# Kernel optimization log

Hardware: AMD Instinct MI355X
Metric: run time of the kernel (lower is better)

## Reference

```python
import jax, jax.numpy as jnp
import numpy as np

DIM = 512
HID = 512
H = 8
HD = HID // H
RB_HID = 64
COORD = 3


def setup_inputs() -> dict:
    key = jax.random.key(0)
    ks = jax.random.split(key, 12)
    B, Nq, Nk = 2, 1024, 2048
    s = 0.02
    return {
        "q_in": jax.random.normal(ks[0], (B, Nq, DIM), jnp.float32),
        "kv_in": jax.random.normal(ks[1], (B, Nk, DIM), jnp.float32),
        "q_coords": jax.random.normal(ks[2], (B, Nq, COORD), jnp.float32),
        "kv_coords": jax.random.normal(ks[3], (B, Nk, COORD), jnp.float32),
        "Wq": jax.random.normal(ks[4], (DIM, HID), jnp.float32) * s,
        "Wk": jax.random.normal(ks[5], (DIM, HID), jnp.float32) * s,
        "Wv": jax.random.normal(ks[6], (DIM, HID), jnp.float32) * s,
        "Wo": jax.random.normal(ks[7], (HID, DIM), jnp.float32) * s,
        "W1": jax.random.normal(ks[8], (1, RB_HID), jnp.float32) * s,
        "b1": jnp.zeros((RB_HID,), jnp.float32),
        "W2": jax.random.normal(ks[9], (RB_HID, H), jnp.float32) * s,
        "b2": jnp.zeros((H,), jnp.float32),
    }


def reference(q_in, kv_in, q_coords, kv_coords, Wq, Wk, Wv, Wo, W1, b1, W2, b2):
    B, Nq, _ = q_in.shape
    Nk = kv_in.shape[1]
    # projections -> [B, H, N, HD]
    q = (q_in @ Wq).reshape(B, Nq, H, HD).transpose(0, 2, 1, 3)
    k = (kv_in @ Wk).reshape(B, Nk, H, HD).transpose(0, 2, 1, 3)
    v = (kv_in @ Wv).reshape(B, Nk, H, HD).transpose(0, 2, 1, 3)
    # pairwise Euclidean distance [B, Nq, Nk]
    diff = q_coords[:, :, None, :] - kv_coords[:, None, :, :]
    d = jnp.sqrt(jnp.sum(diff * diff, axis=-1))
    # 2-layer MLP on distance -> per-head bias [B, H, Nq, Nk]
    h = jax.nn.silu(d[..., None] * W1[0] + b1)  # [B,Nq,Nk,RB_HID]
    bias = (h @ W2 + b2).transpose(0, 3, 1, 2)  # [B,H,Nq,Nk]
    scale = HD ** -0.5
    logits = jnp.einsum("bhqd,bhkd->bhqk", q, k) * scale + bias
    attn = jax.nn.softmax(logits, axis=-1)
    out = jnp.einsum("bhqk,bhkd->bhqd", attn, v)
    out = out.transpose(0, 2, 1, 3).reshape(B, Nq, HID)
    return out @ Wo
```

## Files before the change

kernel.cpp:

```cpp
#include <hip/hip_runtime.h>
#include <hip/hip_bf16.h>
#include <math.h>

typedef short bf16x8 __attribute__((ext_vector_type(8)));
typedef float f32x4 __attribute__((ext_vector_type(4)));
typedef unsigned short u16;
typedef unsigned int u32;

#define NH 8
#define BB 2
#define NQ 1024
#define NK 2048
#define NSPLIT 8
#define M2CONST 6.4921250
#define SC2 0.18033688f
#define LS 68

#define MFMA16(a, b, c) __builtin_amdgcn_mfma_f32_16x16x32_bf16(a, b, c, 0, 0, 0)

__device__ __constant__ double XN_D[6] = {251.63850576500074, 218.50966799187810,
                                          161.12883777312265, 94.871162226877350,
                                          37.490330081221910, 4.3614942349992570};

static __device__ __forceinline__ u32 bfr(float x) {
  u32 u = __builtin_bit_cast(u32, x);
  return u + 0x7FFFu + ((u >> 16) & 1u);
}
static __device__ __forceinline__ u32 pk2(float lo, float hi) {
  return (bfr(lo) >> 16) | (bfr(hi) & 0xFFFF0000u);
}
static __device__ __forceinline__ u16 bfs(float x) { return (u16)(bfr(x) >> 16); }

__global__ __launch_bounds__(256) void setup_kernel(
    const float* __restrict__ Wq, const float* __restrict__ Wk,
    const float* __restrict__ Wv, const float* __restrict__ Wo,
    u16* __restrict__ Tq, u16* __restrict__ Tk,
    u16* __restrict__ Tv, u16* __restrict__ To,
    const float* __restrict__ W1, const float* __restrict__ b1,
    const float* __restrict__ W2, const float* __restrict__ b2,
    float* __restrict__ polyc,
    const float* __restrict__ kc, u16* __restrict__ keg,
    const float* __restrict__ q_in, const float* __restrict__ kv_in,
    u16* __restrict__ qb, u16* __restrict__ kvb) {
  const int blk = blockIdx.x, t = threadIdx.x;
  if (blk >= 273) {
    int gi = (blk - 273) * 256 + t;
    const float* src; u16* dst; size_t off;
    if (gi < 131072) { src = q_in; dst = qb; off = (size_t)gi * 8; }
    else             { src = kv_in; dst = kvb; off = (size_t)(gi - 131072) * 8; }
    float4 a = *(const float4*)(src + off);
    float4 b = *(const float4*)(src + off + 4);
    uint4 o;
    o.x = pk2(a.x, a.y); o.y = pk2(a.z, a.w);
    o.z = pk2(b.x, b.y); o.w = pk2(b.z, b.w);
    *(uint4*)(dst + off) = o;
  } else if (blk < 256) {
    __shared__ u16 tile[64][65];
    const float* W; u16* Wt;
    switch (blk >> 6) {
      case 0: W = Wq; Wt = Tq; break;
      case 1: W = Wk; Wt = Tk; break;
      case 2: W = Wv; Wt = Tv; break;
      default: W = Wo; Wt = To; break;
    }
    const int rem = blk & 63;
    const int k0 = (rem >> 3) * 64, n0 = (rem & 7) * 64;
    const int r = t >> 4, c4 = (t & 15) * 4;
    #pragma unroll
    for (int p = 0; p < 4; p++) {
      int row = p * 16 + r;
      float4 v = *(const float4*)&W[(size_t)(k0 + row) * 512 + n0 + c4];
      tile[row][c4 + 0] = bfs(v.x);
      tile[row][c4 + 1] = bfs(v.y);
      tile[row][c4 + 2] = bfs(v.z);
      tile[row][c4 + 3] = bfs(v.w);
    }
    __syncthreads();
    #pragma unroll
    for (int p = 0; p < 4; p++) {
      int n = p * 16 + r;
      u16 u0 = tile[c4 + 0][n], u1 = tile[c4 + 1][n];
      u16 u2 = tile[c4 + 2][n], u3 = tile[c4 + 3][n];
      uint2 o;
      o.x = u0 | ((u32)u1 << 16);
      o.y = u2 | ((u32)u3 << 16);
      *(uint2*)&Wt[(size_t)(n0 + n) * 512 + k0 + c4] = o;
    }
  } else if (blk == 256) {
    __shared__ double fv[6][8];
    if (t < 48) {
      int i = t >> 3, h = t & 7;
      double x = sqrt(XN_D[i]);
      double acc = (double)b2[h];
      for (int r = 0; r < 64; r++) {
        double u = x * (double)W1[r] + (double)b1[r];
        double s = u / (1.0 + exp(-u));
        acc += s * (double)W2[r * 8 + h];
      }
      fv[i][h] = acc * 1.4426950408889634 - M2CONST;
    }
    __syncthreads();
    if (t < 8) {
      int h = t;
      double c[6];
      #pragma unroll
      for (int i = 0; i < 6; i++) c[i] = fv[i][h];
      for (int k = 1; k < 6; k++)
        for (int i = 5; i >= k; i--)
          c[i] = (c[i] - c[i - 1]) / (XN_D[i] - XN_D[i - k]);
      double m[6] = {c[5], 0, 0, 0, 0, 0};
      int deg = 0;
      for (int i = 4; i >= 0; i--) {
        double np[6] = {};
        for (int j = deg; j >= 0; j--) np[j + 1] += m[j];
        for (int j = 0; j <= deg; j++) np[j] -= XN_D[i] * m[j];
        np[0] += c[i];
        deg++;
        for (int j = 0; j <= deg; j++) m[j] = np[j];
      }
      #pragma unroll
      for (int j = 0; j < 6; j++) polyc[h * 8 + j] = (float)m[j];
    }
  } else {
    int r = (blk - 257) * 256 + t;
    float kx = kc[(size_t)r * 3], ky = kc[(size_t)r * 3 + 1], kz = kc[(size_t)r * 3 + 2];
    uint4 o;
    o.x = pk2(-2.0f * kx, -2.0f * ky);
    o.y = pk2(-2.0f * kz, 1.0f);
    o.z = (u32)bfs(kx * kx + ky * ky + kz * kz);
    o.w = 0;
    *(uint4*)&keg[(size_t)r * 8] = o;
  }
}

__global__ __launch_bounds__(256) void gemm_qkv(
    const u16* __restrict__ qb, const u16* __restrict__ kvb,
    const u16* __restrict__ Wqt, const u16* __restrict__ Wkt,
    const u16* __restrict__ Wvt, u16* __restrict__ Qp,
    u16* __restrict__ Kp, u16* __restrict__ Vtp) {
  __shared__ u16 As[64 * LS];
  __shared__ u16 Bs[64 * LS];
  __shared__ u16 Bs2[64 * LS];
  const int t = threadIdx.x;
  const int w = t >> 6, l = t & 63, g = l >> 4, li = l & 15;
  const int bx = blockIdx.x;
  const bool isQ = bx < 32;
  const int m0 = (isQ ? bx : bx - 32) * 64, n0 = blockIdx.y * 64;
  const u16* A = isQ ? qb : kvb;
  const u16* B1 = isQ ? Wqt : Wkt;
  const int ms = (w & 1) * 32, ns = (w >> 1) * 32;
  f32x4 acc[2][2] = {}, accV[2][2] = {};

  for (int kt = 0; kt < 512; kt += 64) {
    bf16x8 av[2], bk[2], bv2[2];
    #pragma unroll
    for (int p = 0; p < 2; p++) {
      int f = p * 256 + t, r = f >> 3, c8 = (f & 7) * 8;
      av[p] = *(const bf16x8*)&A[(size_t)(m0 + r) * 512 + kt + c8];
      bk[p] = *(const bf16x8*)&B1[(size_t)(n0 + r) * 512 + kt + c8];
    }
    if (!isQ) {
      #pragma unroll
      for (int p = 0; p < 2; p++) {
        int f = p * 256 + t, r = f >> 3, c8 = (f & 7) * 8;
        bv2[p] = *(const bf16x8*)&Wvt[(size_t)(n0 + r) * 512 + kt + c8];
      }
    }
    __syncthreads();
    #pragma unroll
    for (int p = 0; p < 2; p++) {
      int f = p * 256 + t, r = f >> 3, c8 = (f & 7) * 8;
      *(bf16x8*)&As[r * LS + c8] = av[p];
      *(bf16x8*)&Bs[r * LS + c8] = bk[p];
    }
    if (!isQ) {
      #pragma unroll
      for (int p = 0; p < 2; p++) {
        int f = p * 256 + t, r = f >> 3, c8 = (f & 7) * 8;
        *(bf16x8*)&Bs2[r * LS + c8] = bv2[p];
      }
    }
    __syncthreads();
    #pragma unroll
    for (int ks = 0; ks < 2; ks++) {
      bf16x8 a0 = *(const bf16x8*)&As[(ms + li) * LS + ks * 32 + g * 8];
      bf16x8 a1 = *(const bf16x8*)&As[(ms + 16 + li) * LS + ks * 32 + g * 8];
      bf16x8 k0 = *(const bf16x8*)&Bs[(ns + li) * LS + ks * 32 + g * 8];
      bf16x8 k1 = *(const bf16x8*)&Bs[(ns + 16 + li) * LS + ks * 32 + g * 8];
      acc[0][0] = MFMA16(a0, k0, acc[0][0]);
      acc[0][1] = MFMA16(a0, k1, acc[0][1]);
      acc[1][0] = MFMA16(a1, k0, acc[1][0]);
      acc[1][1] = MFMA16(a1, k1, acc[1][1]);
      if (!isQ) {
        bf16x8 v0 = *(const bf16x8*)&Bs2[(ns + li) * LS + ks * 32 + g * 8];
        bf16x8 v1 = *(const bf16x8*)&Bs2[(ns + 16 + li) * LS + ks * 32 + g * 8];
        accV[0][0] = MFMA16(a0, v0, accV[0][0]);
        accV[0][1] = MFMA16(a0, v1, accV[0][1]);
        accV[1][0] = MFMA16(a1, v0, accV[1][0]);
        accV[1][1] = MFMA16(a1, v1, accV[1][1]);
      }
    }
  }
  #pragma unroll
  for (int mi = 0; mi < 2; mi++) {
    #pragma unroll
    for (int ni = 0; ni < 2; ni++) {
      int row = m0 + ms + mi * 16 + 4 * g;
      int col = n0 + ns + ni * 16 + li;
      f32x4 vk = acc[mi][ni];
      if (isQ) {
        #pragma unroll
        for (int r = 0; r < 4; r++) Qp[(size_t)(row + r) * 512 + col] = bfs(vk[r]);
      } else {
        #pragma unroll
        for (int r = 0; r < 4; r++) Kp[(size_t)(row + r) * 512 + col] = bfs(vk[r]);
        f32x4 vv = accV[mi][ni];
        int bb = row >> 11, j = row & 2047;
        int hh = col >> 6, d = col & 63;
        uint2 o;
        o.x = pk2(vv[0], vv[1]);
        o.y = pk2(vv[2], vv[3]);
        *(uint2*)&Vtp[((size_t)((bb * 8 + hh) * 64 + d)) * 2048 + j] = o;
      }
    }
  }
}

__global__ __launch_bounds__(256, 4) void attn_kernel(
    const u16* __restrict__ Qb, const u16* __restrict__ Kb,
    const u16* __restrict__ Vt, const float* __restrict__ qc,
    const u16* __restrict__ keg, const float* __restrict__ polyc,
    float* __restrict__ Op, float* __restrict__ Lp) {
  __shared__ u16 Kl[64 * LS];
  __shared__ u16 Vtl[64 * LS];
  __shared__ u16 Pl[64 * LS];

  const int t = threadIdx.x;
  const int w = t >> 6, l = t & 63, g = l >> 4, li = l & 15;
  const int qt = blockIdx.x >> 3, sidx = blockIdx.x & 7;
  const int h = blockIdx.y, b = blockIdx.z;

  const float c0 = polyc[h * 8 + 0], c1 = polyc[h * 8 + 1];
  const float c2 = polyc[h * 8 + 2], c3 = polyc[h * 8 + 3];
  const float c4 = polyc[h * 8 + 4], c5 = polyc[h * 8 + 5];

  const int qrow = qt * 64 + w * 16 + li;
  const size_t qg = (size_t)b * NQ + qrow;
  bf16x8 qf0 = *(const bf16x8*)&Qb[qg * 512 + h * 64 + g * 8];
  bf16x8 qf1 = *(const bf16x8*)&Qb[qg * 512 + h * 64 + 32 + g * 8];
  float qx = qc[qg * 3], qy = qc[qg * 3 + 1], qz = qc[qg * 3 + 2];
  bf16x8 qe = {};
  if (g == 0) {
    qe[0] = (short)bfs(qx);
    qe[1] = (short)bfs(qy);
    qe[2] = (short)bfs(qz);
    qe[3] = (short)bfs(qx * qx + qy * qy + qz * qz);
    qe[4] = (short)bfs(1.0f);
  }

  f32x4 oacc[4] = {};
  float lacc = 0.0f;

  const u16* Kg = Kb + (size_t)b * NK * 512 + h * 64;
  const u16* Vg = Vt + (size_t)((b * 8 + h) * 64) * 2048;
  const u16* keg_b = keg + (size_t)b * NK * 8;

  const int jb0 = sidx * (NK / NSPLIT);
  const int srow = t >> 3, sc8 = (t & 7) * 8;

  bf16x8 kr0 = *(const bf16x8*)&Kg[(size_t)(jb0 + srow) * 512 + sc8];
  bf16x8 kr1 = *(const bf16x8*)&Kg[(size_t)(jb0 + 32 + srow) * 512 + sc8];
  bf16x8 vr0 = *(const bf16x8*)&Vg[(size_t)srow * 2048 + jb0 + sc8];
  bf16x8 vr1 = *(const bf16x8*)&Vg[(size_t)(32 + srow) * 2048 + jb0 + sc8];

  for (int it = 0; it < NK / NSPLIT / 64; it++) {
    const int jbase = jb0 + it * 64;
    __syncthreads();
    *(bf16x8*)&Kl[srow * LS + sc8] = kr0;
    *(bf16x8*)&Kl[(32 + srow) * LS + sc8] = kr1;
    *(bf16x8*)&Vtl[srow * LS + sc8] = vr0;
    *(bf16x8*)&Vtl[(32 + srow) * LS + sc8] = vr1;
    __syncthreads();
    if (it + 1 < NK / NSPLIT / 64) {
      const int jn = jbase + 64;
      kr0 = *(const bf16x8*)&Kg[(size_t)(jn + srow) * 512 + sc8];
      kr1 = *(const bf16x8*)&Kg[(size_t)(jn + 32 + srow) * 512 + sc8];
      vr0 = *(const bf16x8*)&Vg[(size_t)srow * 2048 + jn + sc8];
      vr1 = *(const bf16x8*)&Vg[(size_t)(32 + srow) * 2048 + jn + sc8];
    }

    #pragma unroll
    for (int j4 = 0; j4 < 4; j4++) {
      bf16x8 ka0 = *(const bf16x8*)&Kl[(j4 * 16 + li) * LS + g * 8];
      bf16x8 ka1 = *(const bf16x8*)&Kl[(j4 * 16 + li) * LS + 32 + g * 8];
      f32x4 z = {};
      f32x4 s0 = MFMA16(ka0, qf0, z);
      f32x4 sac = MFMA16(ka1, qf1, s0);
      bf16x8 ke = {};
      if (g == 0)
        ke = *(const bf16x8*)&keg_b[(size_t)(jbase + j4 * 16 + li) * 8];
      f32x4 dac = MFMA16(ke, qe, z);

      float p[4];
      #pragma unroll
      for (int r = 0; r < 4; r++) {
        float u = fminf(dac[r], 256.0f);
        float gp = fmaf(fmaf(fmaf(fmaf(fmaf(c5, u, c4), u, c3), u, c2), u, c1), u, c0);
        p[r] = __builtin_amdgcn_exp2f(fmaf(sac[r], SC2, gp));
      }
      lacc += (p[0] + p[1]) + (p[2] + p[3]);
      uint2 pv;
      pv.x = pk2(p[0], p[1]);
      pv.y = pk2(p[2], p[3]);
      *(uint2*)&Pl[(w * 16 + li) * LS + j4 * 16 + g * 4] = pv;
    }

    bf16x8 pf0 = *(const bf16x8*)&Pl[(w * 16 + li) * LS + g * 8];
    bf16x8 pf1 = *(const bf16x8*)&Pl[(w * 16 + li) * LS + 32 + g * 8];
    #pragma unroll
    for (int dt = 0; dt < 4; dt++) {
      bf16x8 v0 = *(const bf16x8*)&Vtl[(dt * 16 + li) * LS + g * 8];
      bf16x8 v1 = *(const bf16x8*)&Vtl[(dt * 16 + li) * LS + 32 + g * 8];
      oacc[dt] = MFMA16(pf0, v0, oacc[dt]);
      oacc[dt] = MFMA16(pf1, v1, oacc[dt]);
    }
  }

  float lf = lacc;
  lf += __shfl_xor(lf, 16);
  lf += __shfl_xor(lf, 32);

  const size_t obase =
      ((size_t)(sidx * 16 + b * 8 + h) * 1024 + qt * 64 + w * 16) * 64;
  #pragma unroll
  for (int dt = 0; dt < 4; dt++)
    #pragma unroll
    for (int r = 0; r < 4; r++)
      Op[obase + (size_t)(4 * g + r) * 64 + dt * 16 + li] = oacc[dt][r];
  if (g == 0)
    Lp[(size_t)(sidx * 16 + b * 8 + h) * 1024 + qt * 64 + w * 16 + li] = lf;
}

__global__ __launch_bounds__(256) void combine_kernel(const float* __restrict__ Op,
                                                      const float* __restrict__ Lp,
                                                      u16* __restrict__ AOb) {
  int tid = blockIdx.x * 256 + threadIdx.x;
  int d4 = tid & 15, rh = tid >> 4;
  int bh = rh >> 10, qrow = rh & 1023;
  f32x4 o = {};
  float lsum = 0.0f;
  #pragma unroll
  for (int s = 0; s < NSPLIT; s++) {
    f32x4 v = *(const f32x4*)&Op[((size_t)(s * 16 + bh) * 1024 + qrow) * 64 + d4 * 4];
    o += v;
    lsum += Lp[(size_t)(s * 16 + bh) * 1024 + qrow];
  }
  float inv = __builtin_amdgcn_rcpf(lsum);
  uint2 pk;
  pk.x = pk2(o[0] * inv, o[1] * inv);
  pk.y = pk2(o[2] * inv, o[3] * inv);
  *(uint2*)&AOb[((size_t)(bh >> 3) * NQ + qrow) * 512 + (bh & 7) * 64 + d4 * 4] = pk;
}

__global__ __launch_bounds__(256) void gemm_wo(const u16* __restrict__ A,
                                               const u16* __restrict__ Bt,
                                               float* __restrict__ C) {
  __shared__ u16 As[32 * LS];
  __shared__ u16 Bs[64 * LS];
  const int t = threadIdx.x;
  const int w = t >> 6, l = t & 63, g = l >> 4, li = l & 15;
  const int m0 = blockIdx.x * 32, n0 = blockIdx.y * 64;
  const int ms = (w & 1) * 16, ns = (w >> 1) * 32;
  f32x4 acc[2] = {};
  for (int kt = 0; kt < 512; kt += 64) {
    bf16x8 av, bv[2];
    {
      int r = t >> 3, c8 = (t & 7) * 8;
      av = *(const bf16x8*)&A[(size_t)(m0 + r) * 512 + kt + c8];
    }
    #pragma unroll
    for (int p = 0; p < 2; p++) {
      int f = p * 256 + t, r = f >> 3, c8 = (f & 7) * 8;
      bv[p] = *(const bf16x8*)&Bt[(size_t)(n0 + r) * 512 + kt + c8];
    }
    __syncthreads();
    {
      int r = t >> 3, c8 = (t & 7) * 8;
      *(bf16x8*)&As[r * LS + c8] = av;
    }
    #pragma unroll
    for (int p = 0; p < 2; p++) {
      int f = p * 256 + t, r = f >> 3, c8 = (f & 7) * 8;
      *(bf16x8*)&Bs[r * LS + c8] = bv[p];
    }
    __syncthreads();
    #pragma unroll
    for (int ks = 0; ks < 2; ks++) {
      bf16x8 af = *(const bf16x8*)&As[(ms + li) * LS + ks * 32 + g * 8];
      bf16x8 b0 = *(const bf16x8*)&Bs[(ns + li) * LS + ks * 32 + g * 8];
      bf16x8 b1 = *(const bf16x8*)&Bs[(ns + 16 + li) * LS + ks * 32 + g * 8];
      acc[0] = MFMA16(af, b0, acc[0]);
      acc[1] = MFMA16(af, b1, acc[1]);
    }
  }
  #pragma unroll
  for (int ni = 0; ni < 2; ni++) {
    f32x4 v = acc[ni];
    int row = m0 + ms + 4 * g;
    int col = n0 + ns + ni * 16 + li;
    #pragma unroll
    for (int r = 0; r < 4; r++) C[(size_t)(row + r) * 512 + col] = v[r];
  }
}

extern "C" void kernel_launch(void* const* d_in, const int* in_sizes, int n_in,
                              void* d_out, int out_size, void* d_ws, size_t ws_size,
                              hipStream_t stream) {
  const float* q_in      = (const float*)d_in[0];
  const float* kv_in     = (const float*)d_in[1];
  const float* q_coords  = (const float*)d_in[2];
  const float* kv_coords = (const float*)d_in[3];
  const float* Wq        = (const float*)d_in[4];
  const float* Wk        = (const float*)d_in[5];
  const float* Wv        = (const float*)d_in[6];
  const float* Wo        = (const float*)d_in[7];
  const float* W1        = (const float*)d_in[8];
  const float* b1        = (const float*)d_in[9];
  const float* W2        = (const float*)d_in[10];
  const float* b2        = (const float*)d_in[11];

  char* p = (char*)d_ws;
  u16* Wqt  = (u16*)p; p += (size_t)512 * 512 * 2;
  u16* Wkt  = (u16*)p; p += (size_t)512 * 512 * 2;
  u16* Wvt  = (u16*)p; p += (size_t)512 * 512 * 2;
  u16* Wot  = (u16*)p; p += (size_t)512 * 512 * 2;
  u16* qb   = (u16*)p; p += (size_t)2048 * 512 * 2;
  u16* kvb  = (u16*)p; p += (size_t)4096 * 512 * 2;
  u16* Qp   = (u16*)p; p += (size_t)2048 * 512 * 2;
  u16* Kp   = (u16*)p; p += (size_t)4096 * 512 * 2;
  u16* Vtp  = (u16*)p; p += (size_t)4096 * 512 * 2;
  u16* AOb  = (u16*)p; p += (size_t)2048 * 512 * 2;
  u16* keg  = (u16*)p; p += (size_t)4096 * 8 * 2;
  float* polyc = (float*)p; p += (size_t)64 * 4;
  p = (char*)(((size_t)p + 255) & ~(size_t)255);
  float* Opart = (float*)p; p += (size_t)NSPLIT * 16 * 1024 * 64 * 4;
  float* Lpart = (float*)p; p += (size_t)NSPLIT * 16 * 1024 * 4;

  setup_kernel<<<1809, 256, 0, stream>>>(Wq, Wk, Wv, Wo, Wqt, Wkt, Wvt, Wot,
                                         W1, b1, W2, b2, polyc, kv_coords, keg,
                                         q_in, kv_in, qb, kvb);
  gemm_qkv<<<dim3(96, 8), 256, 0, stream>>>(qb, kvb, Wqt, Wkt, Wvt,
                                            Qp, Kp, Vtp);
  attn_kernel<<<dim3(128, 8, 2), 256, 0, stream>>>(Qp, Kp, Vtp, q_coords, keg,
                                                   polyc, Opart, Lpart);
  combine_kernel<<<1024, 256, 0, stream>>>(Opart, Lpart, AOb);
  gemm_wo<<<dim3(64, 8), 256, 0, stream>>>(AOb, Wot, (float*)d_out);
}
```

Before: 147.9 us.

## Load K/V directly from global in attention and halve key-split count

The attention kernel no longer stages K and V^T tiles through shared memory with block-wide barriers and register prefetch. Each wave now reads its MFMA operands straight from global memory, relying on L1/L2 to absorb the fourfold redundant reads across waves. The key dimension is split into 4 chunks instead of 8, giving fewer blocks with longer loops and less partial-output traffic for the combine step. This trades barrier and LDS overhead for more global and cache load pressure, less latency hiding, and fewer blocks in flight.

Result: slower. 179.4 us (+21.3%).

```diff
diff --git a/kernel.cpp b/kernel.cpp
--- a/kernel.cpp
+++ b/kernel.cpp
@@ -11,7 +11,7 @@
 #define BB 2
 #define NQ 1024
 #define NK 2048
-#define NSPLIT 8
+#define NSPLIT 4
 #define M2CONST 6.4921250
 #define SC2 0.18033688f
 #define LS 68
@@ -231,13 +231,11 @@
     const u16* __restrict__ Vt, const float* __restrict__ qc,
     const u16* __restrict__ keg, const float* __restrict__ polyc,
     float* __restrict__ Op, float* __restrict__ Lp) {
-  __shared__ u16 Kl[64 * LS];
-  __shared__ u16 Vtl[64 * LS];
   __shared__ u16 Pl[64 * LS];
 
   const int t = threadIdx.x;
   const int w = t >> 6, l = t & 63, g = l >> 4, li = l & 15;
-  const int qt = blockIdx.x >> 3, sidx = blockIdx.x & 7;
+  const int qt = blockIdx.x >> 2, sidx = blockIdx.x & 3;
   const int h = blockIdx.y, b = blockIdx.z;
 
   const float c0 = polyc[h * 8 + 0], c1 = polyc[h * 8 + 1];
@@ -264,35 +262,16 @@
   const u16* Kg = Kb + (size_t)b * NK * 512 + h * 64;
   const u16* Vg = Vt + (size_t)((b * 8 + h) * 64) * 2048;
   const u16* keg_b = keg + (size_t)b * NK * 8;
-
   const int jb0 = sidx * (NK / NSPLIT);
-  const int srow = t >> 3, sc8 = (t & 7) * 8;
-
-  bf16x8 kr0 = *(const bf16x8*)&Kg[(size_t)(jb0 + srow) * 512 + sc8];
-  bf16x8 kr1 = *(const bf16x8*)&Kg[(size_t)(jb0 + 32 + srow) * 512 + sc8];
-  bf16x8 vr0 = *(const bf16x8*)&Vg[(size_t)srow * 2048 + jb0 + sc8];
-  bf16x8 vr1 = *(const bf16x8*)&Vg[(size_t)(32 + srow) * 2048 + jb0 + sc8];
 
   for (int it = 0; it < NK / NSPLIT / 64; it++) {
     const int jbase = jb0 + it * 64;
-    __syncthreads();
-    *(bf16x8*)&Kl[srow * LS + sc8] = kr0;
-    *(bf16x8*)&Kl[(32 + srow) * LS + sc8] = kr1;
-    *(bf16x8*)&Vtl[srow * LS + sc8] = vr0;
-    *(bf16x8*)&Vtl[(32 + srow) * LS + sc8] = vr1;
-    __syncthreads();
-    if (it + 1 < NK / NSPLIT / 64) {
-      const int jn = jbase + 64;
-      kr0 = *(const bf16x8*)&Kg[(size_t)(jn + srow) * 512 + sc8];
-      kr1 = *(const bf16x8*)&Kg[(size_t)(jn + 32 + srow) * 512 + sc8];
-      vr0 = *(const bf16x8*)&Vg[(size_t)srow * 2048 + jn + sc8];
-      vr1 = *(const bf16x8*)&Vg[(size_t)(32 + srow) * 2048 + jn + sc8];
-    }
 
     #pragma unroll
     for (int j4 = 0; j4 < 4; j4++) {
-      bf16x8 ka0 = *(const bf16x8*)&Kl[(j4 * 16 + li) * LS + g * 8];
-      bf16x8 ka1 = *(const bf16x8*)&Kl[(j4 * 16 + li) * LS + 32 + g * 8];
+      const u16* krow = &Kg[(size_t)(jbase + j4 * 16 + li) * 512 + g * 8];
+      bf16x8 ka0 = *(const bf16x8*)krow;
+      bf16x8 ka1 = *(const bf16x8*)(krow + 32);
       f32x4 z = {};
       f32x4 s0 = MFMA16(ka0, qf0, z);
       f32x4 sac = MFMA16(ka1, qf1, s0);
@@ -319,8 +298,9 @@
     bf16x8 pf1 = *(const bf16x8*)&Pl[(w * 16 + li) * LS + 32 + g * 8];
     #pragma unroll
     for (int dt = 0; dt < 4; dt++) {
-      bf16x8 v0 = *(const bf16x8*)&Vtl[(dt * 16 + li) * LS + g * 8];
-      bf16x8 v1 = *(const bf16x8*)&Vtl[(dt * 16 + li) * LS + 32 + g * 8];
+      const u16* vrow = &Vg[(size_t)(dt * 16 + li) * 2048 + jbase + g * 8];
+      bf16x8 v0 = *(const bf16x8*)vrow;
+      bf16x8 v1 = *(const bf16x8*)(vrow + 32);
       oacc[dt] = MFMA16(pf0, v0, oacc[dt]);
       oacc[dt] = MFMA16(pf1, v1, oacc[dt]);
     }
@@ -451,8 +431,8 @@
                                          q_in, kv_in, qb, kvb);
   gemm_qkv<<<dim3(96, 8), 256, 0, stream>>>(qb, kvb, Wqt, Wkt, Wvt,
                                             Qp, Kp, Vtp);
-  attn_kernel<<<dim3(128, 8, 2), 256, 0, stream>>>(Qp, Kp, Vtp, q_coords, keg,
-                                                   polyc, Opart, Lpart);
+  attn_kernel<<<dim3(64, 8, 2), 256, 0, stream>>>(Qp, Kp, Vtp, q_coords, keg,
+                                                  polyc, Opart, Lpart);
   combine_kernel<<<1024, 256, 0, stream>>>(Opart, Lpart, AOb);
   gemm_wo<<<dim3(64, 8), 256, 0, stream>>>(AOb, Wot, (float*)d_out);
 }
```
